# Kernel optimization log

Measured on AMD Instinct MI355X. Metric: run time of the kernel, lower is better.

Reference implementation:

```python
import jax, jax.numpy as jnp
import numpy as np

D_MODEL = 1024
N_HEAD = 16


def setup_inputs() -> dict:
    key = jax.random.key(0)
    ks = jax.random.split(key, 11)
    B, S, D = 2, 2048, D_MODEL
    s = 1.0 / np.sqrt(D)
    inp = {
        "q": jax.random.normal(ks[0], (B, S, D), jnp.float32),
        "k": jax.random.normal(ks[1], (B, S, D), jnp.float32),
        "v": jax.random.normal(ks[2], (B, S, D), jnp.float32),
        "Wq": jax.random.normal(ks[3], (D, D), jnp.float32) * s,
        "bq": jnp.zeros((D,), jnp.float32),
        "Wk": jax.random.normal(ks[4], (D, D), jnp.float32) * s,
        "bk": jnp.zeros((D,), jnp.float32),
        "Wv": jax.random.normal(ks[5], (D, D), jnp.float32) * s,
        "bv": jnp.zeros((D,), jnp.float32),
        "Wo": jax.random.normal(ks[6], (D, D), jnp.float32) * s,
        "bo": jnp.zeros((D,), jnp.float32),
    }
    return inp


def _split(x, n_head):
    B, S, D = x.shape
    return x.reshape(B, S, n_head, D // n_head).transpose(0, 2, 1, 3)  # [B,H,S,dh]


def reference(q, k, v, Wq, bq, Wk, bk, Wv, bv, Wo, bo):
    # Linear projections (torch Linear: x @ W.T + b), add_noise=False path
    qh = _split(q @ Wq.T + bq, N_HEAD)
    kh = _split(k @ Wk.T + bk, N_HEAD)
    vh = _split(v @ Wv.T + bv, N_HEAD)
    d_tensor = qh.shape[-1]
    # score = q @ k^T / sqrt(d_tensor); mask=None
    score = jnp.einsum('bhqd,bhkd->bhqk', qh, kh) / jnp.sqrt(jnp.float32(d_tensor))
    attn = jax.nn.softmax(score, axis=-1)
    out = jnp.einsum('bhqk,bhkd->bhqd', attn, vh)
    B, H, S, dh = out.shape
    out = out.transpose(0, 2, 1, 3).reshape(B, S, H * dh)
    return out @ Wo.T + bo
```

## Files before the change

### kernel.cpp

```cpp
#include <hip/hip_runtime.h>
#include <stdint.h>

typedef unsigned short u16;
typedef short bfx8 __attribute__((ext_vector_type(8)));
typedef float fx4 __attribute__((ext_vector_type(4)));

#define B_  2
#define S_  2048
#define D_  1024
#define H_  16
#define DH  64
#define K_  1024
#define M_ROWS 4096
#define QSCALE 0.18033688011112042f


__device__ __forceinline__ u16 f2bf(float x) {
  union { float f; uint32_t u; } c; c.f = x;
  uint32_t r = (c.u + 0x7FFFu + ((c.u >> 16) & 1u)) >> 16;
  return (u16)r;
}

__device__ __forceinline__ fx4 mfma16(bfx8 a, bfx8 b, fx4 c) {
  return __builtin_amdgcn_mfma_f32_16x16x32_bf16(a, b, c, 0, 0, 0);
}

typedef const __attribute__((address_space(1))) void as1_cvoid;
typedef __attribute__((address_space(3))) void as3_void;

__device__ __forceinline__ void stage16(const void* g, void* l) {
  __builtin_amdgcn_global_load_lds((as1_cvoid*)g, (as3_void*)l, 16, 0, 0);
}

__device__ __forceinline__ bfx8 lds_frag(const u16* base, int row, int kelem) {
  int off = (row << 7) + (kelem << 1);
  off ^= (row & 7) << 4;
  return *reinterpret_cast<const bfx8*>(reinterpret_cast<const char*>(base) + off);
}

__device__ __forceinline__ uint32_t cvt_pk_bf16(float lo, float hi) {
  uint32_t r;
  asm("v_cvt_pk_bf16_f32 %0, %1, %2" : "=v"(r) : "v"(lo), "v"(hi));
  return r;
}

__device__ __forceinline__ float exp2_raw(float x) {
  float r;
  asm("v_exp_f32 %0, %1" : "=v"(r) : "v"(x));
  return r;
}


__global__ __launch_bounds__(256) void convert_kernel(
    const float* __restrict__ q, const float* __restrict__ k, const float* __restrict__ v,
    const float* __restrict__ wq, const float* __restrict__ wk, const float* __restrict__ wv,
    const float* __restrict__ wo,
    u16* __restrict__ qb, u16* __restrict__ kb, u16* __restrict__ vb,
    u16* __restrict__ wqb, u16* __restrict__ wkb, u16* __restrict__ wvb,
    u16* __restrict__ wob) {
  const float* s; u16* d; int n8;
  switch (blockIdx.y) {
    case 0: s = q;  d = qb;  n8 = (M_ROWS * D_) / 8; break;
    case 1: s = k;  d = kb;  n8 = (M_ROWS * D_) / 8; break;
    case 2: s = v;  d = vb;  n8 = (M_ROWS * D_) / 8; break;
    case 3: s = wq; d = wqb; n8 = (D_ * D_) / 8; break;
    case 4: s = wk; d = wkb; n8 = (D_ * D_) / 8; break;
    case 5: s = wv; d = wvb; n8 = (D_ * D_) / 8; break;
    default: s = wo; d = wob; n8 = (D_ * D_) / 8; break;
  }
  int idx = blockIdx.x * blockDim.x + threadIdx.x;
  if (idx >= n8) return;
  const float4* sp = reinterpret_cast<const float4*>(s) + (size_t)idx * 2;
  float4 a = sp[0], b = sp[1];
  bfx8 r;
  r[0] = (short)f2bf(a.x); r[1] = (short)f2bf(a.y);
  r[2] = (short)f2bf(a.z); r[3] = (short)f2bf(a.w);
  r[4] = (short)f2bf(b.x); r[5] = (short)f2bf(b.y);
  r[6] = (short)f2bf(b.z); r[7] = (short)f2bf(b.w);
  *reinterpret_cast<bfx8*>(d + (size_t)idx * 8) = r;
}


__device__ __forceinline__ void gemm_core(const u16* __restrict__ A,
                                          const u16* __restrict__ Bt,
                                          int m0, int n0,
                                          u16* Al, u16* Bl, fx4 (&acc)[4][2]) {
  const int tid = threadIdx.x;
  const int lane = tid & 63;
  const int w = tid >> 6;
  const int wr = (w >> 1) << 6;
  const int wc = (w & 1) << 5;
  const int l8 = lane >> 3;
  const int c8 = lane & 7;
  const int fr = lane & 15;
  const int fk = (lane >> 4) << 3;

  for (int k0 = 0; k0 < K_; k0 += 64) {
    #pragma unroll
    for (int i = 0; i < 4; ++i) {
      int j = (w << 2) + i;
      int row = (j << 3) + l8;
      int sc = c8 ^ (row & 7);
      stage16(A + (size_t)(m0 + row) * K_ + k0 + (sc << 3), Al + (j << 9));
    }
    #pragma unroll
    for (int i = 0; i < 2; ++i) {
      int j = (w << 1) + i;
      int row = (j << 3) + l8;
      int sc = c8 ^ (row & 7);
      stage16(Bt + (size_t)(n0 + row) * K_ + k0 + (sc << 3), Bl + (j << 9));
    }
    __syncthreads();
    #pragma unroll
    for (int kb = 0; kb < 2; ++kb) {
      bfx8 af[4], bff[2];
      #pragma unroll
      for (int rb = 0; rb < 4; ++rb)
        af[rb] = lds_frag(Al, wr + rb * 16 + fr, kb * 32 + fk);
      #pragma unroll
      for (int cb = 0; cb < 2; ++cb)
        bff[cb] = lds_frag(Bl, wc + cb * 16 + fr, kb * 32 + fk);
      #pragma unroll
      for (int rb = 0; rb < 4; ++rb)
        #pragma unroll
        for (int cb = 0; cb < 2; ++cb)
          acc[rb][cb] = mfma16(af[rb], bff[cb], acc[rb][cb]);
    }
    __syncthreads();
  }
}


__global__ __launch_bounds__(256, 2) void proj_gemm(
    const u16* __restrict__ qb, const u16* __restrict__ kb, const u16* __restrict__ vb,
    const u16* __restrict__ wqb, const u16* __restrict__ wkb, const u16* __restrict__ wvb,
    const float* __restrict__ bq, const float* __restrict__ bk, const float* __restrict__ bv,
    u16* __restrict__ Qh, u16* __restrict__ Kh, u16* __restrict__ VT) {
  __shared__ alignas(16) u16 Al[128 * 64];
  __shared__ alignas(16) u16 Bl[64 * 64];
  int bid = blockIdx.x;
  int z = bid >> 9;
  int t = bid & 511;
  const u16 *A, *Bt; const float* bias;
  if (z == 0)      { A = qb;  Bt = wqb; bias = bq; }
  else if (z == 1) { A = kb;  Bt = wkb; bias = bk; }
  else             { A = wvb; Bt = vb;  bias = bv; }
  int m0, n0;
  if (z < 2) { m0 = (t >> 4) << 7; n0 = (t & 15) << 6; }
  else       { m0 = (t >> 6) << 7; n0 = (t & 63) << 6; }

  fx4 acc[4][2];
  #pragma unroll
  for (int i = 0; i < 4; ++i)
    #pragma unroll
    for (int j = 0; j < 2; ++j) acc[i][j] = (fx4){0.f, 0.f, 0.f, 0.f};

  gemm_core(A, Bt, m0, n0, Al, Bl, acc);

  const int lane = threadIdx.x & 63;
  const int w = threadIdx.x >> 6;
  const int wr = (w >> 1) << 6, wc = (w & 1) << 5;
  const int fr = lane & 15;
  const int rq = (lane >> 4) << 2;

  if (z < 2) {
    u16* O = (z == 0) ? Qh : Kh;
    float scale = (z == 0) ? QSCALE : 1.0f;
    #pragma unroll
    for (int cb = 0; cb < 2; ++cb) {
      int n = n0 + wc + cb * 16 + fr;
      float bn = bias[n];
      int h = n >> 6, dd = n & 63;
      #pragma unroll
      for (int rb = 0; rb < 4; ++rb) {
        #pragma unroll
        for (int r = 0; r < 4; ++r) {
          int m = m0 + wr + rb * 16 + rq + r;
          int b = m >> 11, srow = m & 2047;
          O[((size_t)((b * H_ + h) * S_ + srow) << 6) + dd] =
              f2bf((acc[rb][cb][r] + bn) * scale);
        }
      }
    }
  } else {
    #pragma unroll
    for (int rb = 0; rb < 4; ++rb) {
      #pragma unroll
      for (int r = 0; r < 4; ++r) {
        int m = m0 + wr + rb * 16 + rq + r;
        float bm = bias[m];
        int h = m >> 6, dd = m & 63;
        #pragma unroll
        for (int cb = 0; cb < 2; ++cb) {
          int n = n0 + wc + cb * 16 + fr;
          int b = n >> 11, srow = n & 2047;
          VT[(size_t)((b * H_ + h) * DH + dd) * S_ + srow] =
              f2bf(acc[rb][cb][r] + bm);
        }
      }
    }
  }
}


__global__ __launch_bounds__(512, 4) void attn_kernel(
    const u16* __restrict__ Qh, const u16* __restrict__ Kh,
    const u16* __restrict__ VT, u16* __restrict__ AO) {
  __shared__ alignas(16) u16 Klds[2][64 * 64];
  __shared__ alignas(16) u16 Vlds[2][64 * 64];

  const int blk = ((blockIdx.x & 7) << 6) + (blockIdx.x >> 3);
  const int bh = blk >> 4;
  const int qt = blk & 15;
  const int tid = threadIdx.x;
  const int lane = tid & 63;
  const int w = tid >> 6;
  const int q0 = (qt << 7) + (w << 4);
  const int c = lane & 15;
  const int g = lane >> 4;
  const int l8 = lane >> 3;
  const int c8 = lane & 7;
  const int sc = c8 ^ l8;
  const size_t base = (size_t)bh * (S_ * DH);
  const u16* Qp = Qh + base;
  const u16* Kp = Kh + base;
  const u16* Vp = VT + base;
  const int b = bh >> 4, h = bh & 15;

  bfx8 qf[2];
  #pragma unroll
  for (int kbi = 0; kbi < 2; ++kbi)
    qf[kbi] = *reinterpret_cast<const bfx8*>(
        Qp + (size_t)(q0 + c) * DH + kbi * 32 + (g << 3));

  fx4 acc[4];
  #pragma unroll
  for (int db = 0; db < 4; ++db) acc[db] = (fx4){0.f, 0.f, 0.f, 0.f};
  float m_ = 0.f, l_ = 0.f;

#define STAGE(bufi, kv0s)                                                       \
  do {                                                                          \
    stage16(Kp + (size_t)((kv0s) + (w << 3) + l8) * DH + (sc << 3),             \
            &Klds[bufi][w << 9]);                                               \
    stage16(Vp + (size_t)((w << 3) + l8) * S_ + (kv0s) + (sc << 3),             \
            &Vlds[bufi][w << 9]);                                               \
  } while (0)

  STAGE(0, 0);
  __syncthreads();

  for (int t = 0; t < S_ / 64; ++t) {
    const int cur = t & 1;
    if (t < S_ / 64 - 1) STAGE(cur ^ 1, (t + 1) * 64);

    fx4 sf[4];
    #pragma unroll
    for (int cb = 0; cb < 4; ++cb) sf[cb] = (fx4){0.f, 0.f, 0.f, 0.f};
    __builtin_amdgcn_s_setprio(1);
    #pragma unroll
    for (int kbi = 0; kbi < 2; ++kbi) {
      bfx8 kf[4];
      #pragma unroll
      for (int cb = 0; cb < 4; ++cb)
        kf[cb] = lds_frag(&Klds[cur][0], cb * 16 + c, kbi * 32 + (g << 3));
      #pragma unroll
      for (int cb = 0; cb < 4; ++cb)
        sf[cb] = mfma16(kf[cb], qf[kbi], sf[cb]);
    }
    __builtin_amdgcn_s_setprio(0);

    float mx = sf[0][0];
    #pragma unroll
    for (int cb = 0; cb < 4; ++cb)
      #pragma unroll
      for (int r = 0; r < 4; ++r) mx = fmaxf(mx, sf[cb][r]);

    if (t == 0) {
      mx = fmaxf(mx, __shfl_xor(mx, 16));
      mx = fmaxf(mx, __shfl_xor(mx, 32));
      m_ = mx;
    } else if (__any(mx - m_ > 14.f)) {
      mx = fmaxf(mx, __shfl_xor(mx, 16));
      mx = fmaxf(mx, __shfl_xor(mx, 32));
      float mnew = fmaxf(m_, mx);
      float alpha = exp2_raw(m_ - mnew);
      l_ *= alpha;
      float ab[4];
      #pragma unroll
      for (int r = 0; r < 4; ++r)
        ab[r] = __shfl(alpha, (lane & 48) + (g << 2) + r);
      #pragma unroll
      for (int db = 0; db < 4; ++db)
        #pragma unroll
        for (int r = 0; r < 4; ++r) acc[db][r] *= ab[r];
      m_ = mnew;
    }

    float p[4][4];
    float rs = 0.f;
    #pragma unroll
    for (int cb = 0; cb < 4; ++cb)
      #pragma unroll
      for (int r = 0; r < 4; ++r) {
        p[cb][r] = exp2_raw(sf[cb][r] - m_);
        rs += p[cb][r];
      }
    l_ += rs;

    uint32_t E[2][2][2];
    #pragma unroll
    for (int cb = 0; cb < 4; ++cb)
      #pragma unroll
      for (int hh = 0; hh < 2; ++hh)
        E[cb >> 1][cb & 1][hh] = cvt_pk_bf16(p[cb][2 * hh], p[cb][2 * hh + 1]);
    #pragma unroll
    for (int r2 = 0; r2 < 2; ++r2)
      #pragma unroll
      for (int r0 = 0; r0 < 2; ++r0) {
        asm("v_permlane32_swap_b32 %0, %1"
            : "+v"(E[r2][0][r0]), "+v"(E[r2][1][r0]));
        asm("v_permlane16_swap_b32 %0, %1"
            : "+v"(E[r2][0][r0]), "+v"(E[r2][1][r0]));
      }

    __builtin_amdgcn_s_setprio(1);
    #pragma unroll
    for (int kbi = 0; kbi < 2; ++kbi) {
      bfx8 vf[4];
      #pragma unroll
      for (int db = 0; db < 4; ++db)
        vf[db] = lds_frag(&Vlds[cur][0], db * 16 + c, kbi * 32 + (g << 3));
      union { uint32_t wd[4]; bfx8 v; } pu;
      pu.wd[0] = E[kbi][0][0]; pu.wd[1] = E[kbi][0][1];
      pu.wd[2] = E[kbi][1][0]; pu.wd[3] = E[kbi][1][1];
      #pragma unroll
      for (int db = 0; db < 4; ++db)
        acc[db] = mfma16(pu.v, vf[db], acc[db]);
    }
    __builtin_amdgcn_s_setprio(0);

    __syncthreads();
  }
#undef STAGE

  l_ += __shfl_xor(l_, 16);
  l_ += __shfl_xor(l_, 32);
  float linv = 1.0f / l_;
  float invb[4];
  #pragma unroll
  for (int r = 0; r < 4; ++r)
    invb[r] = __shfl(linv, (lane & 48) + (g << 2) + r);
  #pragma unroll
  for (int db = 0; db < 4; ++db)
    #pragma unroll
    for (int r = 0; r < 4; ++r) {
      int qrow = q0 + (g << 2) + r;
      AO[(size_t)(b * S_ + qrow) * D_ + h * DH + db * 16 + c] =
          f2bf(acc[db][r] * invb[r]);
    }
}


__global__ __launch_bounds__(256, 2) void out_gemm(
    const u16* __restrict__ AO, const u16* __restrict__ wob,
    const float* __restrict__ bo, float* __restrict__ out) {
  __shared__ alignas(16) u16 Al[128 * 64];
  __shared__ alignas(16) u16 Bl[64 * 64];
  int t = blockIdx.x;
  int m0 = (t >> 4) << 7, n0 = (t & 15) << 6;
  fx4 acc[4][2];
  #pragma unroll
  for (int i = 0; i < 4; ++i)
    #pragma unroll
    for (int j = 0; j < 2; ++j) acc[i][j] = (fx4){0.f, 0.f, 0.f, 0.f};
  gemm_core(AO, wob, m0, n0, Al, Bl, acc);
  const int lane = threadIdx.x & 63;
  const int w = threadIdx.x >> 6;
  const int wr = (w >> 1) << 6, wc = (w & 1) << 5;
  #pragma unroll
  for (int cb = 0; cb < 2; ++cb) {
    int n = n0 + wc + cb * 16 + (lane & 15);
    float bn = bo[n];
    #pragma unroll
    for (int rb = 0; rb < 4; ++rb)
      #pragma unroll
      for (int r = 0; r < 4; ++r) {
        int m = m0 + wr + rb * 16 + ((lane >> 4) << 2) + r;
        out[(size_t)m * D_ + n] = acc[rb][cb][r] + bn;
      }
  }
}


extern "C" void kernel_launch(void* const* d_in, const int* in_sizes, int n_in,
                              void* d_out, int out_size, void* d_ws, size_t ws_size,
                              hipStream_t stream) {
  (void)in_sizes; (void)n_in; (void)out_size;
  const size_t MB = 1024 * 1024;
  if (ws_size < 56 * MB) return;

  const float* q  = (const float*)d_in[0];
  const float* k  = (const float*)d_in[1];
  const float* v  = (const float*)d_in[2];
  const float* Wq = (const float*)d_in[3];
  const float* bq = (const float*)d_in[4];
  const float* Wk = (const float*)d_in[5];
  const float* bk = (const float*)d_in[6];
  const float* Wv = (const float*)d_in[7];
  const float* bv = (const float*)d_in[8];
  const float* Wo = (const float*)d_in[9];
  const float* bo = (const float*)d_in[10];
  float* out = (float*)d_out;

  char* ws = (char*)d_ws;
  u16* qb  = (u16*)(ws);
  u16* kb  = (u16*)(ws + 8 * MB);
  u16* vb  = (u16*)(ws + 16 * MB);
  u16* wqb = (u16*)(ws + 24 * MB);
  u16* wkb = (u16*)(ws + 26 * MB);
  u16* wvb = (u16*)(ws + 28 * MB);
  u16* wob = (u16*)(ws + 30 * MB);
  u16* Qh  = (u16*)(ws + 32 * MB);
  u16* Kh  = (u16*)(ws + 40 * MB);
  u16* VT  = (u16*)(ws + 48 * MB);
  u16* AO  = qb;

  convert_kernel<<<dim3(2048, 7), 256, 0, stream>>>(q, k, v, Wq, Wk, Wv, Wo,
                                                    qb, kb, vb, wqb, wkb, wvb, wob);
  proj_gemm<<<1536, 256, 0, stream>>>(qb, kb, vb, wqb, wkb, wvb, bq, bk, bv, Qh, Kh, VT);
  attn_kernel<<<512, 512, 0, stream>>>(Qh, Kh, VT, AO);
  out_gemm<<<512, 256, 0, stream>>>(AO, wob, bo, out);
}
```

Measured before the change: 227.5 us.

## Enlarge GEMM tiles with double-buffered LDS, shrink attention blocks, use MFMA row sums

The projection and output GEMMs move from 128x64 to 128x128 tiles with double-buffered LDS staging, prefetching the next K slice during compute, XCD-aware block remapping, and raised wave priority. The attention kernel goes from 512 to 256 threads with 64-row query tiles, doubling the grid. It computes the softmax denominator with an extra MFMA against a ones vector instead of scalar sums and shuffles, and takes the row max with a three-input max tree. Larger tiles cut global reloads but use more LDS and registers and launch fewer blocks, which can hurt occupancy.

```diff
diff --git a/kernel.cpp b/kernel.cpp
--- a/kernel.cpp
+++ b/kernel.cpp
@@ -48,6 +48,10 @@
   float r;
   asm("v_exp_f32 %0, %1" : "=v"(r) : "v"(x));
   return r;
+}
+
+__device__ __forceinline__ float max3f(float a, float b, float c) {
+  return fmaxf(fmaxf(a, b), c);
 }
 
 
@@ -81,51 +85,55 @@
 }
 
 
-__device__ __forceinline__ void gemm_core(const u16* __restrict__ A,
-                                          const u16* __restrict__ Bt,
-                                          int m0, int n0,
-                                          u16* Al, u16* Bl, fx4 (&acc)[4][2]) {
-  const int tid = threadIdx.x;
-  const int lane = tid & 63;
-  const int w = tid >> 6;
-  const int wr = (w >> 1) << 6;
-  const int wc = (w & 1) << 5;
-  const int l8 = lane >> 3;
-  const int c8 = lane & 7;
-  const int fr = lane & 15;
-  const int fk = (lane >> 4) << 3;
-
-  for (int k0 = 0; k0 < K_; k0 += 64) {
-    #pragma unroll
-    for (int i = 0; i < 4; ++i) {
-      int j = (w << 2) + i;
-      int row = (j << 3) + l8;
-      int sc = c8 ^ (row & 7);
-      stage16(A + (size_t)(m0 + row) * K_ + k0 + (sc << 3), Al + (j << 9));
-    }
-    #pragma unroll
-    for (int i = 0; i < 2; ++i) {
-      int j = (w << 1) + i;
-      int row = (j << 3) + l8;
-      int sc = c8 ^ (row & 7);
-      stage16(Bt + (size_t)(n0 + row) * K_ + k0 + (sc << 3), Bl + (j << 9));
-    }
-    __syncthreads();
+__device__ __forceinline__ void g128_stage(const u16* __restrict__ A,
+                                           const u16* __restrict__ Bt,
+                                           int m0, int n0, int k0,
+                                           u16* Ad, u16* Bd,
+                                           int w, int l8, int c8) {
+  #pragma unroll
+  for (int i = 0; i < 4; ++i) {
+    int j = (w << 2) + i;
+    int row = (j << 3) + l8;
+    int sc = c8 ^ (row & 7);
+    stage16(A + (size_t)(m0 + row) * K_ + k0 + (sc << 3), Ad + (j << 9));
+    stage16(Bt + (size_t)(n0 + row) * K_ + k0 + (sc << 3), Bd + (j << 9));
+  }
+}
+
+__device__ __forceinline__ void gemm128_core(const u16* __restrict__ A,
+                                             const u16* __restrict__ Bt,
+                                             int m0, int n0,
+                                             u16 (*Al)[128 * 64], u16 (*Bl)[128 * 64],
+                                             fx4 (&acc)[4][4]) {
+  const int lane = threadIdx.x & 63;
+  const int w = threadIdx.x >> 6;
+  const int l8 = lane >> 3, c8 = lane & 7;
+  const int fr = lane & 15, fk = (lane >> 4) << 3;
+  const int wr = (w >> 1) << 6, wc = (w & 1) << 6;
+
+  g128_stage(A, Bt, m0, n0, 0, Al[0], Bl[0], w, l8, c8);
+  __syncthreads();
+  for (int t = 0; t < K_ / 64; ++t) {
+    const int cur = t & 1;
+    if (t + 1 < K_ / 64)
+      g128_stage(A, Bt, m0, n0, (t + 1) * 64, Al[cur ^ 1], Bl[cur ^ 1], w, l8, c8);
+    __builtin_amdgcn_s_setprio(1);
     #pragma unroll
     for (int kb = 0; kb < 2; ++kb) {
-      bfx8 af[4], bff[2];
+      bfx8 af[4], bf[4];
       #pragma unroll
       for (int rb = 0; rb < 4; ++rb)
-        af[rb] = lds_frag(Al, wr + rb * 16 + fr, kb * 32 + fk);
-      #pragma unroll
-      for (int cb = 0; cb < 2; ++cb)
-        bff[cb] = lds_frag(Bl, wc + cb * 16 + fr, kb * 32 + fk);
+        af[rb] = lds_frag(Al[cur], wr + rb * 16 + fr, kb * 32 + fk);
+      #pragma unroll
+      for (int cb = 0; cb < 4; ++cb)
+        bf[cb] = lds_frag(Bl[cur], wc + cb * 16 + fr, kb * 32 + fk);
       #pragma unroll
       for (int rb = 0; rb < 4; ++rb)
         #pragma unroll
-        for (int cb = 0; cb < 2; ++cb)
-          acc[rb][cb] = mfma16(af[rb], bff[cb], acc[rb][cb]);
-    }
+        for (int cb = 0; cb < 4; ++cb)
+          acc[rb][cb] = mfma16(af[rb], bf[cb], acc[rb][cb]);
+    }
+    __builtin_amdgcn_s_setprio(0);
     __syncthreads();
   }
 }
@@ -136,30 +144,30 @@
     const u16* __restrict__ wqb, const u16* __restrict__ wkb, const u16* __restrict__ wvb,
     const float* __restrict__ bq, const float* __restrict__ bk, const float* __restrict__ bv,
     u16* __restrict__ Qh, u16* __restrict__ Kh, u16* __restrict__ VT) {
-  __shared__ alignas(16) u16 Al[128 * 64];
-  __shared__ alignas(16) u16 Bl[64 * 64];
-  int bid = blockIdx.x;
-  int z = bid >> 9;
-  int t = bid & 511;
+  __shared__ alignas(16) u16 Al[2][128 * 64];
+  __shared__ alignas(16) u16 Bl[2][128 * 64];
+  int bid = (blockIdx.x & 7) * 96 + (blockIdx.x >> 3);
+  int z = bid >> 8;
+  int t = bid & 255;
   const u16 *A, *Bt; const float* bias;
   if (z == 0)      { A = qb;  Bt = wqb; bias = bq; }
   else if (z == 1) { A = kb;  Bt = wkb; bias = bk; }
   else             { A = wvb; Bt = vb;  bias = bv; }
   int m0, n0;
-  if (z < 2) { m0 = (t >> 4) << 7; n0 = (t & 15) << 6; }
-  else       { m0 = (t >> 6) << 7; n0 = (t & 63) << 6; }
-
-  fx4 acc[4][2];
+  if (z < 2) { m0 = (t >> 3) << 7; n0 = (t & 7) << 7; }
+  else       { m0 = (t >> 5) << 7; n0 = (t & 31) << 7; }
+
+  fx4 acc[4][4];
   #pragma unroll
   for (int i = 0; i < 4; ++i)
     #pragma unroll
-    for (int j = 0; j < 2; ++j) acc[i][j] = (fx4){0.f, 0.f, 0.f, 0.f};
-
-  gemm_core(A, Bt, m0, n0, Al, Bl, acc);
+    for (int j = 0; j < 4; ++j) acc[i][j] = (fx4){0.f, 0.f, 0.f, 0.f};
+
+  gemm128_core(A, Bt, m0, n0, Al, Bl, acc);
 
   const int lane = threadIdx.x & 63;
   const int w = threadIdx.x >> 6;
-  const int wr = (w >> 1) << 6, wc = (w & 1) << 5;
+  const int wr = (w >> 1) << 6, wc = (w & 1) << 6;
   const int fr = lane & 15;
   const int rq = (lane >> 4) << 2;
 
@@ -167,7 +175,7 @@
     u16* O = (z == 0) ? Qh : Kh;
     float scale = (z == 0) ? QSCALE : 1.0f;
     #pragma unroll
-    for (int cb = 0; cb < 2; ++cb) {
+    for (int cb = 0; cb < 4; ++cb) {
       int n = n0 + wc + cb * 16 + fr;
       float bn = bias[n];
       int h = n >> 6, dd = n & 63;
@@ -191,7 +199,7 @@
         float bm = bias[m];
         int h = m >> 6, dd = m & 63;
         #pragma unroll
-        for (int cb = 0; cb < 2; ++cb) {
+        for (int cb = 0; cb < 4; ++cb) {
           int n = n0 + wc + cb * 16 + fr;
           int b = n >> 11, srow = n & 2047;
           VT[(size_t)((b * H_ + h) * DH + dd) * S_ + srow] =
@@ -203,19 +211,19 @@
 }
 
 
-__global__ __launch_bounds__(512, 4) void attn_kernel(
+__global__ __launch_bounds__(256, 4) void attn_kernel(
     const u16* __restrict__ Qh, const u16* __restrict__ Kh,
     const u16* __restrict__ VT, u16* __restrict__ AO) {
   __shared__ alignas(16) u16 Klds[2][64 * 64];
   __shared__ alignas(16) u16 Vlds[2][64 * 64];
 
-  const int blk = ((blockIdx.x & 7) << 6) + (blockIdx.x >> 3);
-  const int bh = blk >> 4;
-  const int qt = blk & 15;
+  const int blk = ((blockIdx.x & 7) << 7) + (blockIdx.x >> 3);
+  const int bh = blk >> 5;
+  const int qt = blk & 31;
   const int tid = threadIdx.x;
   const int lane = tid & 63;
   const int w = tid >> 6;
-  const int q0 = (qt << 7) + (w << 4);
+  const int q0 = (qt << 6) + (w << 4);
   const int c = lane & 15;
   const int g = lane >> 4;
   const int l8 = lane >> 3;
@@ -233,17 +241,27 @@
     qf[kbi] = *reinterpret_cast<const bfx8*>(
         Qp + (size_t)(q0 + c) * DH + kbi * 32 + (g << 3));
 
+  bfx8 ones;
+  #pragma unroll
+  for (int i = 0; i < 8; ++i) ones[i] = (short)0x3F80;
+
   fx4 acc[4];
   #pragma unroll
   for (int db = 0; db < 4; ++db) acc[db] = (fx4){0.f, 0.f, 0.f, 0.f};
-  float m_ = 0.f, l_ = 0.f;
+  fx4 accl = (fx4){0.f, 0.f, 0.f, 0.f};
+  float m_ = 0.f;
 
 #define STAGE(bufi, kv0s)                                                       \
   do {                                                                          \
-    stage16(Kp + (size_t)((kv0s) + (w << 3) + l8) * DH + (sc << 3),             \
-            &Klds[bufi][w << 9]);                                               \
-    stage16(Vp + (size_t)((w << 3) + l8) * S_ + (kv0s) + (sc << 3),             \
-            &Vlds[bufi][w << 9]);                                               \
+    _Pragma("unroll")                                                           \
+    for (int i = 0; i < 2; ++i) {                                               \
+      int j = (w << 1) + i;                                                     \
+      int row = (j << 3) + l8;                                                  \
+      stage16(Kp + (size_t)((kv0s) + row) * DH + (sc << 3),                     \
+              &Klds[bufi][j << 9]);                                             \
+      stage16(Vp + (size_t)row * S_ + (kv0s) + (sc << 3),                       \
+              &Vlds[bufi][j << 9]);                                             \
+    }                                                                           \
   } while (0)
 
   STAGE(0, 0);
@@ -269,11 +287,12 @@
     }
     __builtin_amdgcn_s_setprio(0);
 
-    float mx = sf[0][0];
-    #pragma unroll
-    for (int cb = 0; cb < 4; ++cb)
-      #pragma unroll
-      for (int r = 0; r < 4; ++r) mx = fmaxf(mx, sf[cb][r]);
+    float t0 = max3f(sf[0][0], sf[0][1], sf[0][2]);
+    float t1 = max3f(sf[0][3], sf[1][0], sf[1][1]);
+    float t2 = max3f(sf[1][2], sf[1][3], sf[2][0]);
+    float t3 = max3f(sf[2][1], sf[2][2], sf[2][3]);
+    float t4 = max3f(sf[3][0], sf[3][1], sf[3][2]);
+    float mx = fmaxf(max3f(t0, t1, t2), max3f(t3, t4, sf[3][3]));
 
     if (t == 0) {
       mx = fmaxf(mx, __shfl_xor(mx, 16));
@@ -284,7 +303,6 @@
       mx = fmaxf(mx, __shfl_xor(mx, 32));
       float mnew = fmaxf(m_, mx);
       float alpha = exp2_raw(m_ - mnew);
-      l_ *= alpha;
       float ab[4];
       #pragma unroll
       for (int r = 0; r < 4; ++r)
@@ -293,19 +311,17 @@
       for (int db = 0; db < 4; ++db)
         #pragma unroll
         for (int r = 0; r < 4; ++r) acc[db][r] *= ab[r];
+      #pragma unroll
+      for (int r = 0; r < 4; ++r) accl[r] *= ab[r];
       m_ = mnew;
     }
 
     float p[4][4];
-    float rs = 0.f;
     #pragma unroll
     for (int cb = 0; cb < 4; ++cb)
       #pragma unroll
-      for (int r = 0; r < 4; ++r) {
+      for (int r = 0; r < 4; ++r)
         p[cb][r] = exp2_raw(sf[cb][r] - m_);
-        rs += p[cb][r];
-      }
-    l_ += rs;
 
     uint32_t E[2][2][2];
     #pragma unroll
@@ -336,6 +352,7 @@
       #pragma unroll
       for (int db = 0; db < 4; ++db)
         acc[db] = mfma16(pu.v, vf[db], acc[db]);
+      accl = mfma16(pu.v, ones, accl);
     }
     __builtin_amdgcn_s_setprio(0);
 
@@ -343,13 +360,9 @@
   }
 #undef STAGE
 
-  l_ += __shfl_xor(l_, 16);
-  l_ += __shfl_xor(l_, 32);
-  float linv = 1.0f / l_;
   float invb[4];
   #pragma unroll
-  for (int r = 0; r < 4; ++r)
-    invb[r] = __shfl(linv, (lane & 48) + (g << 2) + r);
+  for (int r = 0; r < 4; ++r) invb[r] = 1.0f / accl[r];
   #pragma unroll
   for (int db = 0; db < 4; ++db)
     #pragma unroll
@@ -364,21 +377,21 @@
 __global__ __launch_bounds__(256, 2) void out_gemm(
     const u16* __restrict__ AO, const u16* __restrict__ wob,
     const float* __restrict__ bo, float* __restrict__ out) {
-  __shared__ alignas(16) u16 Al[128 * 64];
-  __shared__ alignas(16) u16 Bl[64 * 64];
-  int t = blockIdx.x;
-  int m0 = (t >> 4) << 7, n0 = (t & 15) << 6;
-  fx4 acc[4][2];
+  __shared__ alignas(16) u16 Al[2][128 * 64];
+  __shared__ alignas(16) u16 Bl[2][128 * 64];
+  int t = (blockIdx.x & 7) * 32 + (blockIdx.x >> 3);
+  int m0 = (t >> 3) << 7, n0 = (t & 7) << 7;
+  fx4 acc[4][4];
   #pragma unroll
   for (int i = 0; i < 4; ++i)
     #pragma unroll
-    for (int j = 0; j < 2; ++j) acc[i][j] = (fx4){0.f, 0.f, 0.f, 0.f};
-  gemm_core(AO, wob, m0, n0, Al, Bl, acc);
+    for (int j = 0; j < 4; ++j) acc[i][j] = (fx4){0.f, 0.f, 0.f, 0.f};
+  gemm128_core(AO, wob, m0, n0, Al, Bl, acc);
   const int lane = threadIdx.x & 63;
   const int w = threadIdx.x >> 6;
-  const int wr = (w >> 1) << 6, wc = (w & 1) << 5;
-  #pragma unroll
-  for (int cb = 0; cb < 2; ++cb) {
+  const int wr = (w >> 1) << 6, wc = (w & 1) << 6;
+  #pragma unroll
+  for (int cb = 0; cb < 4; ++cb) {
     int n = n0 + wc + cb * 16 + (lane & 15);
     float bn = bo[n];
     #pragma unroll
@@ -427,7 +440,7 @@
 
   convert_kernel<<<dim3(2048, 7), 256, 0, stream>>>(q, k, v, Wq, Wk, Wv, Wo,
                                                     qb, kb, vb, wqb, wkb, wvb, wob);
-  proj_gemm<<<1536, 256, 0, stream>>>(qb, kb, vb, wqb, wkb, wvb, bq, bk, bv, Qh, Kh, VT);
-  attn_kernel<<<512, 512, 0, stream>>>(Qh, Kh, VT, AO);
-  out_gemm<<<512, 256, 0, stream>>>(AO, wob, bo, out);
-}
+  proj_gemm<<<768, 256, 0, stream>>>(qb, kb, vb, wqb, wkb, wvb, bq, bk, bv, Qh, Kh, VT);
+  attn_kernel<<<1024, 256, 0, stream>>>(Qh, Kh, VT, AO);
+  out_gemm<<<256, 256, 0, stream>>>(AO, wob, bo, out);
+}
```

Result: no change. 227.4 us (-0.1%).
